# Kernel tuning notes

Hardware: AMD Instinct MI355X
Metric: run time of the kernel (lower is better)

The kernel has to match this reference:

```python
import jax, jax.numpy as jnp
import numpy as np

B, T, F, H = 512, 1024, 64, 512  # batch, timesteps, n_features, hidden_dims


def _lstm_cell(x, h, c, W_ih, W_hh, b_ih, b_hh):
    # torch.nn.LSTMCell gate order: i, f, g, o
    g = x @ W_ih.T + b_ih + h @ W_hh.T + b_hh
    i, f, gg, o = jnp.split(g, 4, axis=-1)
    c_new = jax.nn.sigmoid(f) * c + jax.nn.sigmoid(i) * jnp.tanh(gg)
    h_new = jax.nn.sigmoid(o) * jnp.tanh(c_new)
    return h_new, c_new


def setup_inputs() -> dict:
    key = jax.random.key(0)
    ks = jax.random.split(key, 9)
    s1 = 1.0 / np.sqrt(H)  # torch LSTMCell init scale for lstm1
    s2 = 1.0 / np.sqrt(F)  # for lstm2 (hidden size = n_features)
    u = lambda k, shape, s: jax.random.uniform(k, shape, jnp.float32, -s, s)
    return {
        "data": jax.random.normal(ks[0], (B, T * F), jnp.float32),
        "W_ih1": u(ks[1], (4 * H, F), s1),
        "W_hh1": u(ks[2], (4 * H, H), s1),
        "b_ih1": u(ks[3], (4 * H,), s1),
        "b_hh1": u(ks[4], (4 * H,), s1),
        "W_ih2": u(ks[5], (4 * F, H), s2),
        "W_hh2": u(ks[6], (4 * F, F), s2),
        "b_ih2": u(ks[7], (4 * F,), s2),
        "b_hh2": u(ks[8], (4 * F,), s2),
        "future": 0,
    }


def reference(data, W_ih1, W_hh1, b_ih1, b_hh1, W_ih2, W_hh2, b_ih2, b_hh2, future):
    x = data.reshape(B, T, F).transpose(1, 0, 2)  # [T, B, F] for scan
    h1 = jnp.zeros((B, H), data.dtype)
    c1 = jnp.zeros((B, H), data.dtype)
    h2 = jnp.zeros((B, F), data.dtype)
    c2 = jnp.zeros((B, F), data.dtype)  # this is the 'output' in the torch code

    def step(carry, x_t):
        h1, c1, h2, c2 = carry
        h1, c1 = _lstm_cell(x_t, h1, c1, W_ih1, W_hh1, b_ih1, b_hh1)
        # NOTE: original feeds c_t (cell state of lstm1) into lstm2, and the
        # per-step 'output' is lstm2's CELL state c2 (h_t2, output = lstm2(...)).
        h2, c2 = _lstm_cell(c1, h2, c2, W_ih2, W_hh2, b_ih2, b_hh2)
        return (h1, c1, h2, c2), c2

    (h1, c1, h2, c2), outs = jax.lax.scan(step, (h1, c1, h2, c2), x)
    outputs = [outs]  # [T, B, F]
    out_t = c2
    for _ in range(int(future)):  # future is a Python int constant
        h1, c1 = _lstm_cell(out_t, h1, c1, W_ih1, W_hh1, b_ih1, b_hh1)
        h2, out_t = _lstm_cell(c1, h2, out_t, W_ih2, W_hh2, b_ih2, b_hh2)
        outputs.append(out_t[None])
    out = jnp.concatenate(outputs, axis=0).transpose(1, 0, 2)  # [B, T+future, F]
    return jnp.squeeze(out, axis=2) if out.shape[2] == 1 else out
```

## Files before the change

### kernel.cpp

```cpp
#include <hip/hip_runtime.h>

#define Bn   512
#define Tn   1024
#define Fn   64
#define Hn   512
#define NB1  128
#define NB2  16
#define NBLK (NB1 + NB2)
#define GMEM 18
#define TRIES (1L << 22)

typedef short bf16x8 __attribute__((ext_vector_type(8)));
typedef float f32x4  __attribute__((ext_vector_type(4)));

__device__ __forceinline__ short f2bf(float f) {
    union { float f; unsigned u; } v; v.f = f;
    unsigned r = (v.u + 0x7FFFu + ((v.u >> 16) & 1u)) >> 16;
    return (short)(unsigned short)r;
}
__device__ __forceinline__ float sigm(float x) { return 1.f / (1.f + __expf(-x)); }
__device__ __forceinline__ float tanh_(float x) { return 2.f / (1.f + __expf(-2.f * x)) - 1.f; }

__device__ __forceinline__ bf16x8 cvt8(const float* p) {
    const float4 v0 = *(const float4*)p;
    const float4 v1 = *(const float4*)(p + 4);
    bf16x8 a;
    a[0] = f2bf(v0.x); a[1] = f2bf(v0.y); a[2] = f2bf(v0.z); a[3] = f2bf(v0.w);
    a[4] = f2bf(v1.x); a[5] = f2bf(v1.y); a[6] = f2bf(v1.z); a[7] = f2bf(v1.w);
    return a;
}

__device__ __forceinline__ void ldx16(bf16x8& d, const short* p) {
    asm volatile("global_load_dwordx4 %0, %1, off sc0 sc1" : "=v"(d) : "v"(p));
}
__device__ __forceinline__ void stx16(short* p, bf16x8 v) {
    asm volatile("global_store_dwordx4 %0, %1, off sc0 sc1" :: "v"(p), "v"(v) : "memory");
}
#define VMWAIT(N) do { \
    asm volatile("s_waitcnt vmcnt(" #N ")" ::: "memory"); \
    __builtin_amdgcn_sched_barrier(0); } while (0)

__device__ __forceinline__ int aldi(const int* p) {
    return __hip_atomic_load(p, __ATOMIC_RELAXED, __HIP_MEMORY_SCOPE_AGENT);
}

__device__ __forceinline__ void flag_arrive(int* slot, int val) {
    asm volatile("s_waitcnt vmcnt(0)" ::: "memory");
    __builtin_amdgcn_sched_barrier(0);
    __syncthreads();
    if (threadIdx.x == 0)
        __hip_atomic_store(slot, val, __ATOMIC_RELEASE, __HIP_MEMORY_SCOPE_AGENT);
}
__device__ __forceinline__ void flag_wait(const int* flags, int tgtA, int tgtB) {
    const int lane = threadIdx.x & 63;
    const int tgt = (lane < 16) ? tgtA : tgtB;
    long spins = 0;
    for (;;) {
        bool ok = (lane >= GMEM) ||
            (aldi(flags + lane) >= tgt);
        if (__all(ok)) break;
        if (++spins > TRIES) break;
        __builtin_amdgcn_s_sleep(1);
    }
    __atomic_signal_fence(__ATOMIC_ACQUIRE);
    __builtin_amdgcn_sched_barrier(0);
}

__global__ void prep_kernel(const float* __restrict__ Wih1, const float* __restrict__ Whh1,
                            const float* __restrict__ Wih2, const float* __restrict__ Whh2,
                            const float* __restrict__ bih1, const float* __restrict__ bhh1,
                            const float* __restrict__ bih2, const float* __restrict__ bhh2,
                            short* __restrict__ h1g, short* __restrict__ h2g,
                            short* __restrict__ w1f, short* __restrict__ w2f,
                            float* __restrict__ bs1, float* __restrict__ bs2,
                            int* __restrict__ bar) {
    const int i0 = blockIdx.x * blockDim.x + threadIdx.x;
    const int stride = gridDim.x * blockDim.x;
    for (int i = i0; i < 1024; i += stride) bar[i] = 0;
    for (int i = i0; i < 2 * Bn * Hn; i += stride) h1g[i] = 0;
    for (int i = i0; i < 2 * Bn * Fn; i += stride) h2g[i] = 0;
    for (int i = i0; i < 2048 * 576; i += stride) {
        int kk = i & 31, n = (i >> 5) & 15, ct = (i >> 9) & 3;
        int r = i >> 11; int kb = r % 18; int ut = r / 18;
        int gcol = ct * 512 + ut * 16 + n;
        int k = kb * 32 + kk;
        float v = (k < 64) ? Wih1[gcol * 64 + k] : Whh1[gcol * 512 + (k - 64)];
        w1f[i] = f2bf(v);
    }
    for (int i = i0; i < 256 * 576; i += stride) {
        int kk = i & 31, n = (i >> 5) & 15, ct = (i >> 9) & 3;
        int r = i >> 11; int kb = r % 18; int ut4 = r / 18;
        int gcol = ct * 64 + ut4 * 16 + n;
        int k = kb * 32 + kk;
        float v = (k < 512) ? Wih2[gcol * 512 + k] : Whh2[gcol * 64 + (k - 512)];
        w2f[i] = f2bf(v);
    }
    for (int i = i0; i < 2048; i += stride) bs1[i] = bih1[i] + bhh1[i];
    for (int i = i0; i < 256;  i += stride) bs2[i] = bih2[i] + bhh2[i];
}

__global__ __launch_bounds__(256, 1) void lstm_kernel(
    const float* __restrict__ data,
    const short* __restrict__ w1f, const float* __restrict__ bs1,
    const short* __restrict__ w2f, const float* __restrict__ bs2,
    short* __restrict__ h1g, short* __restrict__ c1g, short* __restrict__ h2g,
    float* __restrict__ out, int* __restrict__ bar) {
    extern __shared__ short smem[];
    const int tid = threadIdx.x;
    const int lane = tid & 63, wv = tid >> 6;
    const int n = lane & 15, q = lane >> 4;
    const int wvr = wv & 1, wvc = wv >> 1;
    const int bid = blockIdx.x;
    const f32x4 Z4 = {0.f, 0.f, 0.f, 0.f};
    short* htile = smem + 32768;
    short* ctile = smem + 34816;

    if (bid < NB1) {
        const int rt = bid >> 4, utp = bid & 15;
        const int ut = utp * 2 + wvc;
        const int rowbase = rt * 64 + wvr * 32;
        const int ucol = ut * 16 + n;
        int* grp = bar + rt * 32;
        const float bi_ = bs1[ucol], bf_ = bs1[512 + ucol], bg_ = bs1[1024 + ucol], bo_ = bs1[1536 + ucol];
        const short* wbase = w1f + ut * 36864 + n * 32 + q * 8;
        const int r0 = rowbase + n, r1 = rowbase + 16 + n;
        const int lr0 = wvr * 32 + n, lr1 = lr0 + 16, sw = n & 7;

        bf16x8 wr[16][4];
#pragma unroll
        for (int kb = 0; kb < 16; ++kb)
#pragma unroll
            for (int g = 0; g < 4; ++g)
                wr[kb][g] = *(const bf16x8*)(wbase + ((kb + 2) * 4 + g) * 512);

        f32x4 c1f[2]; c1f[0] = Z4; c1f[1] = Z4;

        for (int t = 0; t < Tn; ++t) {
            const short* h1r = h1g + (t & 1) * (Bn * Hn);
            short* h1w = h1g + ((t + 1) & 1) * (Bn * Hn);
            short* c1w = c1g + (t & 1) * (Bn * Hn);
            f32x4 acc[2][4];
#pragma unroll
            for (int a = 0; a < 2; ++a)
#pragma unroll
                for (int g = 0; g < 4; ++g) acc[a][g] = Z4;

            const float* x0 = data + (size_t)r0 * 65536 + t * 64;
            const float* x1 = data + (size_t)r1 * 65536 + t * 64;
#pragma unroll
            for (int kb = 0; kb < 2; ++kb) {
                const bf16x8 a0 = cvt8(x0 + kb * 32 + q * 8);
                const bf16x8 a1 = cvt8(x1 + kb * 32 + q * 8);
#pragma unroll
                for (int g = 0; g < 4; ++g) {
                    const bf16x8 b = *(const bf16x8*)(wbase + (kb * 4 + g) * 512);
                    acc[0][g] = __builtin_amdgcn_mfma_f32_16x16x32_bf16(a0, b, acc[0][g], 0, 0, 0);
                    acc[1][g] = __builtin_amdgcn_mfma_f32_16x16x32_bf16(a1, b, acc[1][g], 0, 0, 0);
                }
            }

            flag_wait(grp, t, t - 1);

            const short* gsrc = h1r + (size_t)rt * 32768;
            bf16x8 st[16];
            __builtin_amdgcn_sched_barrier(0);
#pragma unroll
            for (int i = 0; i < 16; ++i) {
                const int c = i * 256 + tid;
                ldx16(st[i], gsrc + c * 8);
            }
            VMWAIT(8);
#pragma unroll
            for (int i = 0; i < 8; ++i) {
                const int c = i * 256 + tid; const int row = c >> 6, col = c & 63;
                *(bf16x8*)&smem[row * 512 + ((col ^ (row & 7)) * 8)] = st[i];
            }
            VMWAIT(0);
#pragma unroll
            for (int i = 8; i < 16; ++i) {
                const int c = i * 256 + tid; const int row = c >> 6, col = c & 63;
                *(bf16x8*)&smem[row * 512 + ((col ^ (row & 7)) * 8)] = st[i];
            }
            __syncthreads();

#pragma unroll
            for (int kb = 0; kb < 16; ++kb) {
                const bf16x8 a0 = *(const bf16x8*)&smem[lr0 * 512 + (((kb * 4 + q) ^ sw) * 8)];
                const bf16x8 a1 = *(const bf16x8*)&smem[lr1 * 512 + (((kb * 4 + q) ^ sw) * 8)];
#pragma unroll
                for (int g = 0; g < 4; ++g) {
                    acc[0][g] = __builtin_amdgcn_mfma_f32_16x16x32_bf16(a0, wr[kb][g], acc[0][g], 0, 0, 0);
                    acc[1][g] = __builtin_amdgcn_mfma_f32_16x16x32_bf16(a1, wr[kb][g], acc[1][g], 0, 0, 0);
                }
            }

#pragma unroll
            for (int rt16 = 0; rt16 < 2; ++rt16) {
#pragma unroll
                for (int r = 0; r < 4; ++r) {
                    const float xi = acc[rt16][0][r] + bi_;
                    const float xf = acc[rt16][1][r] + bf_;
                    const float xg = acc[rt16][2][r] + bg_;
                    const float xo = acc[rt16][3][r] + bo_;
                    const float ii = sigm(xi), ff = sigm(xf), gg = tanh_(xg), oo = sigm(xo);
                    const float c = ff * c1f[rt16][r] + ii * gg;
                    c1f[rt16][r] = c;
                    const float h = oo * tanh_(c);
                    const int lr = wvr * 32 + rt16 * 16 + q * 4 + r;
                    const int lu = wvc * 16 + n;
                    htile[lr * 32 + lu] = f2bf(h);
                    ctile[lr * 32 + lu] = f2bf(c);
                }
            }
            __syncthreads();
            {
                const int row = tid >> 2, part = tid & 3;
                const bf16x8 hv = *(const bf16x8*)&htile[row * 32 + part * 8];
                const bf16x8 cv = *(const bf16x8*)&ctile[row * 32 + part * 8];
                short* gdst = h1w + (size_t)(rt * 64 + row) * 512 + utp * 32 + part * 8;
                short* gdc  = c1w + (size_t)(rt * 64 + row) * 512 + utp * 32 + part * 8;
                stx16(gdst, hv);
                stx16(gdc, cv);
            }
            flag_arrive(grp + utp, t + 1);
        }
    } else {
        const int b2 = bid - NB1;
        const int rt2 = b2 >> 1, u2 = b2 & 1;
        const int ut4 = u2 * 2 + wvc;
        const int rowbase = rt2 * 64 + wvr * 32;
        const int ucol = ut4 * 16 + n;
        int* grp = bar + rt2 * 32;
        const float bi_ = bs2[ucol], bf_ = bs2[64 + ucol], bg_ = bs2[128 + ucol], bo_ = bs2[192 + ucol];
        const short* wbase = w2f + ut4 * 36864 + n * 32 + q * 8;
        const int r0 = rowbase + n, r1 = rowbase + 16 + n;
        const int lr0 = wvr * 32 + n, lr1 = lr0 + 16, sw = n & 7;

        bf16x8 wr[16][4];
#pragma unroll
        for (int kb = 0; kb < 16; ++kb)
#pragma unroll
            for (int g = 0; g < 4; ++g)
                wr[kb][g] = *(const bf16x8*)(wbase + (kb * 4 + g) * 512);
        bf16x8 wh[2][4];
#pragma unroll
        for (int kb2 = 0; kb2 < 2; ++kb2)
#pragma unroll
            for (int g = 0; g < 4; ++g)
                wh[kb2][g] = *(const bf16x8*)(wbase + ((16 + kb2) * 4 + g) * 512);

        f32x4 c2f[2]; c2f[0] = Z4; c2f[1] = Z4;

        for (int t = 0; t < Tn; ++t) {
            flag_wait(grp, t + 1, t);
            const short* c1r = c1g + (t & 1) * (Bn * Hn);
            const short* h2r = h2g + (t & 1) * (Bn * Fn);
            short* h2w = h2g + ((t + 1) & 1) * (Bn * Fn);
            f32x4 acc[2][4];
#pragma unroll
            for (int a = 0; a < 2; ++a)
#pragma unroll
                for (int g = 0; g < 4; ++g) acc[a][g] = Z4;

            bf16x8 SH[4];
            __builtin_amdgcn_sched_barrier(0);
            ldx16(SH[0], h2r + (size_t)r0 * 64 + q * 8);
            ldx16(SH[1], h2r + (size_t)r0 * 64 + 32 + q * 8);
            ldx16(SH[2], h2r + (size_t)r1 * 64 + q * 8);
            ldx16(SH[3], h2r + (size_t)r1 * 64 + 32 + q * 8);
            const short* gsrc = c1r + (size_t)rt2 * 32768;
            bf16x8 st[16];
#pragma unroll
            for (int i = 0; i < 16; ++i) {
                const int c = i * 256 + tid;
                ldx16(st[i], gsrc + c * 8);
            }
            VMWAIT(8);
#pragma unroll
            for (int i = 0; i < 8; ++i) {
                const int c = i * 256 + tid; const int row = c >> 6, col = c & 63;
                *(bf16x8*)&smem[row * 512 + ((col ^ (row & 7)) * 8)] = st[i];
            }
            VMWAIT(0);
#pragma unroll
            for (int i = 8; i < 16; ++i) {
                const int c = i * 256 + tid; const int row = c >> 6, col = c & 7 ? (c & 63) : (c & 63);
                const int col2 = c & 63;
                *(bf16x8*)&smem[row * 512 + ((col2 ^ (row & 7)) * 8)] = st[i];
            }
            __syncthreads();

#pragma unroll
            for (int kb = 0; kb < 16; ++kb) {
                const bf16x8 a0 = *(const bf16x8*)&smem[lr0 * 512 + (((kb * 4 + q) ^ sw) * 8)];
                const bf16x8 a1 = *(const bf16x8*)&smem[lr1 * 512 + (((kb * 4 + q) ^ sw) * 8)];
#pragma unroll
                for (int g = 0; g < 4; ++g) {
                    acc[0][g] = __builtin_amdgcn_mfma_f32_16x16x32_bf16(a0, wr[kb][g], acc[0][g], 0, 0, 0);
                    acc[1][g] = __builtin_amdgcn_mfma_f32_16x16x32_bf16(a1, wr[kb][g], acc[1][g], 0, 0, 0);
                }
            }
#pragma unroll
            for (int g = 0; g < 4; ++g) {
                acc[0][g] = __builtin_amdgcn_mfma_f32_16x16x32_bf16(SH[0], wh[0][g], acc[0][g], 0, 0, 0);
                acc[0][g] = __builtin_amdgcn_mfma_f32_16x16x32_bf16(SH[1], wh[1][g], acc[0][g], 0, 0, 0);
                acc[1][g] = __builtin_amdgcn_mfma_f32_16x16x32_bf16(SH[2], wh[0][g], acc[1][g], 0, 0, 0);
                acc[1][g] = __builtin_amdgcn_mfma_f32_16x16x32_bf16(SH[3], wh[1][g], acc[1][g], 0, 0, 0);
            }

#pragma unroll
            for (int rt16 = 0; rt16 < 2; ++rt16) {
#pragma unroll
                for (int r = 0; r < 4; ++r) {
                    const float xi = acc[rt16][0][r] + bi_;
                    const float xf = acc[rt16][1][r] + bf_;
                    const float xg = acc[rt16][2][r] + bg_;
                    const float xo = acc[rt16][3][r] + bo_;
                    const float ii = sigm(xi), ff = sigm(xf), gg = tanh_(xg), oo = sigm(xo);
                    const float c = ff * c2f[rt16][r] + ii * gg;
                    c2f[rt16][r] = c;
                    const float h = oo * tanh_(c);
                    const int row = rowbase + rt16 * 16 + q * 4 + r;
                    out[(size_t)row * 65536 + (size_t)t * 64 + ucol] = c;
                    const int lr = wvr * 32 + rt16 * 16 + q * 4 + r;
                    const int lu = wvc * 16 + n;
                    htile[lr * 32 + lu] = f2bf(h);
                }
            }
            __syncthreads();
            {
                const int row = tid >> 2, part = tid & 3;
                const bf16x8 hv = *(const bf16x8*)&htile[row * 32 + part * 8];
                short* gdst = h2w + (size_t)(rt2 * 64 + row) * 64 + u2 * 32 + part * 8;
                stx16(gdst, hv);
            }
            flag_arrive(grp + 16 + u2, t + 1);
        }
    }
}

extern "C" void kernel_launch(void* const* d_in, const int* in_sizes, int n_in,
                              void* d_out, int out_size, void* d_ws, size_t ws_size,
                              hipStream_t stream) {
    const float* data = (const float*)d_in[0];
    const float* Wih1 = (const float*)d_in[1];
    const float* Whh1 = (const float*)d_in[2];
    const float* bih1 = (const float*)d_in[3];
    const float* bhh1 = (const float*)d_in[4];
    const float* Wih2 = (const float*)d_in[5];
    const float* Whh2 = (const float*)d_in[6];
    const float* bih2 = (const float*)d_in[7];
    const float* bhh2 = (const float*)d_in[8];
    float* out = (float*)d_out;

    char* w = (char*)d_ws;
    short* h1g = (short*)(w + 0);
    short* c1g = (short*)(w + 1048576);
    short* h2g = (short*)(w + 2097152);
    short* w2f = (short*)(w + 2228224);
    short* w1f = (short*)(w + 2523136);
    float* bs1 = (float*)(w + 4882432);
    float* bs2 = (float*)(w + 4890624);
    int* bar  = (int*)(w + 4891648);

    hipLaunchKernelGGL(prep_kernel, dim3(1024), dim3(256), 0, stream,
                       Wih1, Whh1, Wih2, Whh2, bih1, bhh1, bih2, bhh2,
                       h1g, h2g, w1f, w2f, bs1, bs2, bar);

    hipLaunchKernelGGL(lstm_kernel, dim3(NBLK), dim3(256), 73728, stream,
                       data, w1f, bs1, w2f, bs2, h1g, c1g, h2g, out, bar);
}
```

Before: 8.305 ms.

## Repartition LSTM blocks into 16 row groups of 9 with LDS-resident h2

Changes the block decomposition from 8 row groups of 64 rows (16 layer-1 blocks plus 2 layer-2 blocks each) to 16 groups of 32 rows, each with 8 layer-1 blocks and one layer-2 block. The layer-2 block now keeps its hidden state h2 in double-buffered shared memory instead of a global buffer, which removes the global h2 round trip and one internal barrier. Each group now synchronises through 9 flags instead of 18, and per-step h1/c1 tile loads are halved. The trade-off is smaller per-block tiles with the same total block count, and a single layer-2 block per group that handles all 64 output columns.

```diff
diff --git a/kernel.cpp b/kernel.cpp
--- a/kernel.cpp
+++ b/kernel.cpp
@@ -4,10 +4,9 @@
 #define Tn   1024
 #define Fn   64
 #define Hn   512
-#define NB1  128
-#define NB2  16
-#define NBLK (NB1 + NB2)
-#define GMEM 18
+#define NGRP 16
+#define GMEM 9
+#define NBLK (NGRP * GMEM)
 #define TRIES (1L << 22)
 
 typedef short bf16x8 __attribute__((ext_vector_type(8)));
@@ -53,11 +52,10 @@
 }
 __device__ __forceinline__ void flag_wait(const int* flags, int tgtA, int tgtB) {
     const int lane = threadIdx.x & 63;
-    const int tgt = (lane < 16) ? tgtA : tgtB;
+    const int tgt = (lane < 8) ? tgtA : tgtB;
     long spins = 0;
     for (;;) {
-        bool ok = (lane >= GMEM) ||
-            (aldi(flags + lane) >= tgt);
+        bool ok = (lane >= GMEM) || (aldi(flags + lane) >= tgt);
         if (__all(ok)) break;
         if (++spins > TRIES) break;
         __builtin_amdgcn_s_sleep(1);
@@ -103,28 +101,28 @@
     const float* __restrict__ data,
     const short* __restrict__ w1f, const float* __restrict__ bs1,
     const short* __restrict__ w2f, const float* __restrict__ bs2,
-    short* __restrict__ h1g, short* __restrict__ c1g, short* __restrict__ h2g,
+    short* __restrict__ h1g, short* __restrict__ c1g,
     float* __restrict__ out, int* __restrict__ bar) {
     extern __shared__ short smem[];
     const int tid = threadIdx.x;
     const int lane = tid & 63, wv = tid >> 6;
     const int n = lane & 15, q = lane >> 4;
-    const int wvr = wv & 1, wvc = wv >> 1;
+    const int wvc = wv;
     const int bid = blockIdx.x;
+    const int rt = bid / GMEM, role = bid % GMEM;
     const f32x4 Z4 = {0.f, 0.f, 0.f, 0.f};
-    short* htile = smem + 32768;
-    short* ctile = smem + 34816;
-
-    if (bid < NB1) {
-        const int rt = bid >> 4, utp = bid & 15;
-        const int ut = utp * 2 + wvc;
-        const int rowbase = rt * 64 + wvr * 32;
+    const int rowbase = rt * 32;
+    int* grp = bar + rt * 32;
+    short* tile0 = smem + 16384;
+    short* tile1 = smem + 18432;
+    const int r0 = rowbase + n, r1 = rowbase + 16 + n;
+    const int lr0 = n, lr1 = n + 16, sw = n & 7;
+
+    if (role < 8) {
+        const int ut = role * 4 + wvc;
         const int ucol = ut * 16 + n;
-        int* grp = bar + rt * 32;
         const float bi_ = bs1[ucol], bf_ = bs1[512 + ucol], bg_ = bs1[1024 + ucol], bo_ = bs1[1536 + ucol];
         const short* wbase = w1f + ut * 36864 + n * 32 + q * 8;
-        const int r0 = rowbase + n, r1 = rowbase + 16 + n;
-        const int lr0 = wvr * 32 + n, lr1 = lr0 + 16, sw = n & 7;
 
         bf16x8 wr[16][4];
 #pragma unroll
@@ -161,23 +159,20 @@
 
             flag_wait(grp, t, t - 1);
 
-            const short* gsrc = h1r + (size_t)rt * 32768;
-            bf16x8 st[16];
+            const short* gsrc = h1r + (size_t)rt * 16384;
+            bf16x8 st[8];
             __builtin_amdgcn_sched_barrier(0);
 #pragma unroll
-            for (int i = 0; i < 16; ++i) {
-                const int c = i * 256 + tid;
-                ldx16(st[i], gsrc + c * 8);
-            }
-            VMWAIT(8);
-#pragma unroll
-            for (int i = 0; i < 8; ++i) {
+            for (int i = 0; i < 8; ++i) ldx16(st[i], gsrc + (i * 256 + tid) * 8);
+            VMWAIT(4);
+#pragma unroll
+            for (int i = 0; i < 4; ++i) {
                 const int c = i * 256 + tid; const int row = c >> 6, col = c & 63;
                 *(bf16x8*)&smem[row * 512 + ((col ^ (row & 7)) * 8)] = st[i];
             }
             VMWAIT(0);
 #pragma unroll
-            for (int i = 8; i < 16; ++i) {
+            for (int i = 4; i < 8; ++i) {
                 const int c = i * 256 + tid; const int row = c >> 6, col = c & 63;
                 *(bf16x8*)&smem[row * 512 + ((col ^ (row & 7)) * 8)] = st[i];
             }
@@ -206,35 +201,29 @@
                     const float c = ff * c1f[rt16][r] + ii * gg;
                     c1f[rt16][r] = c;
                     const float h = oo * tanh_(c);
-                    const int lr = wvr * 32 + rt16 * 16 + q * 4 + r;
+                    const int lr = rt16 * 16 + q * 4 + r;
                     const int lu = wvc * 16 + n;
-                    htile[lr * 32 + lu] = f2bf(h);
-                    ctile[lr * 32 + lu] = f2bf(c);
+                    tile0[lr * 64 + lu] = f2bf(h);
+                    tile1[lr * 64 + lu] = f2bf(c);
                 }
             }
             __syncthreads();
             {
-                const int row = tid >> 2, part = tid & 3;
-                const bf16x8 hv = *(const bf16x8*)&htile[row * 32 + part * 8];
-                const bf16x8 cv = *(const bf16x8*)&ctile[row * 32 + part * 8];
-                short* gdst = h1w + (size_t)(rt * 64 + row) * 512 + utp * 32 + part * 8;
-                short* gdc  = c1w + (size_t)(rt * 64 + row) * 512 + utp * 32 + part * 8;
+                const int row = tid >> 3, part = tid & 7;
+                const bf16x8 hv = *(const bf16x8*)&tile0[row * 64 + part * 8];
+                const bf16x8 cv = *(const bf16x8*)&tile1[row * 64 + part * 8];
+                short* gdst = h1w + (size_t)(rowbase + row) * 512 + role * 64 + part * 8;
+                short* gdc  = c1w + (size_t)(rowbase + row) * 512 + role * 64 + part * 8;
                 stx16(gdst, hv);
                 stx16(gdc, cv);
             }
-            flag_arrive(grp + utp, t + 1);
+            flag_arrive(grp + role, t + 1);
         }
     } else {
-        const int b2 = bid - NB1;
-        const int rt2 = b2 >> 1, u2 = b2 & 1;
-        const int ut4 = u2 * 2 + wvc;
-        const int rowbase = rt2 * 64 + wvr * 32;
+        const int ut4 = wvc;
         const int ucol = ut4 * 16 + n;
-        int* grp = bar + rt2 * 32;
         const float bi_ = bs2[ucol], bf_ = bs2[64 + ucol], bg_ = bs2[128 + ucol], bo_ = bs2[192 + ucol];
         const short* wbase = w2f + ut4 * 36864 + n * 32 + q * 8;
-        const int r0 = rowbase + n, r1 = rowbase + 16 + n;
-        const int lr0 = wvr * 32 + n, lr1 = lr0 + 16, sw = n & 7;
 
         bf16x8 wr[16][4];
 #pragma unroll
@@ -249,44 +238,38 @@
             for (int g = 0; g < 4; ++g)
                 wh[kb2][g] = *(const bf16x8*)(wbase + ((16 + kb2) * 4 + g) * 512);
 
+        for (int i = tid; i < 2048; i += 256) { tile0[i] = 0; tile1[i] = 0; }
+        __syncthreads();
+
         f32x4 c2f[2]; c2f[0] = Z4; c2f[1] = Z4;
 
         for (int t = 0; t < Tn; ++t) {
             flag_wait(grp, t + 1, t);
             const short* c1r = c1g + (t & 1) * (Bn * Hn);
-            const short* h2r = h2g + (t & 1) * (Bn * Fn);
-            short* h2w = h2g + ((t + 1) & 1) * (Bn * Fn);
+            const short* h2rd = (t & 1) ? tile1 : tile0;
+            short* h2wr = (t & 1) ? tile0 : tile1;
             f32x4 acc[2][4];
 #pragma unroll
             for (int a = 0; a < 2; ++a)
 #pragma unroll
                 for (int g = 0; g < 4; ++g) acc[a][g] = Z4;
 
-            bf16x8 SH[4];
+            const short* gsrc = c1r + (size_t)rt * 16384;
+            bf16x8 st[8];
             __builtin_amdgcn_sched_barrier(0);
-            ldx16(SH[0], h2r + (size_t)r0 * 64 + q * 8);
-            ldx16(SH[1], h2r + (size_t)r0 * 64 + 32 + q * 8);
-            ldx16(SH[2], h2r + (size_t)r1 * 64 + q * 8);
-            ldx16(SH[3], h2r + (size_t)r1 * 64 + 32 + q * 8);
-            const short* gsrc = c1r + (size_t)rt2 * 32768;
-            bf16x8 st[16];
-#pragma unroll
-            for (int i = 0; i < 16; ++i) {
-                const int c = i * 256 + tid;
-                ldx16(st[i], gsrc + c * 8);
-            }
-            VMWAIT(8);
-#pragma unroll
-            for (int i = 0; i < 8; ++i) {
+#pragma unroll
+            for (int i = 0; i < 8; ++i) ldx16(st[i], gsrc + (i * 256 + tid) * 8);
+            VMWAIT(4);
+#pragma unroll
+            for (int i = 0; i < 4; ++i) {
                 const int c = i * 256 + tid; const int row = c >> 6, col = c & 63;
                 *(bf16x8*)&smem[row * 512 + ((col ^ (row & 7)) * 8)] = st[i];
             }
             VMWAIT(0);
 #pragma unroll
-            for (int i = 8; i < 16; ++i) {
-                const int c = i * 256 + tid; const int row = c >> 6, col = c & 7 ? (c & 63) : (c & 63);
-                const int col2 = c & 63;
-                *(bf16x8*)&smem[row * 512 + ((col2 ^ (row & 7)) * 8)] = st[i];
+            for (int i = 4; i < 8; ++i) {
+                const int c = i * 256 + tid; const int row = c >> 6, col = c & 63;
+                *(bf16x8*)&smem[row * 512 + ((col ^ (row & 7)) * 8)] = st[i];
             }
             __syncthreads();
 
@@ -301,11 +284,14 @@
                 }
             }
 #pragma unroll
-            for (int g = 0; g < 4; ++g) {
-                acc[0][g] = __builtin_amdgcn_mfma_f32_16x16x32_bf16(SH[0], wh[0][g], acc[0][g], 0, 0, 0);
-                acc[0][g] = __builtin_amdgcn_mfma_f32_16x16x32_bf16(SH[1], wh[1][g], acc[0][g], 0, 0, 0);
-                acc[1][g] = __builtin_amdgcn_mfma_f32_16x16x32_bf16(SH[2], wh[0][g], acc[1][g], 0, 0, 0);
-                acc[1][g] = __builtin_amdgcn_mfma_f32_16x16x32_bf16(SH[3], wh[1][g], acc[1][g], 0, 0, 0);
+            for (int kb2 = 0; kb2 < 2; ++kb2) {
+                const bf16x8 a0 = *(const bf16x8*)&h2rd[lr0 * 64 + (((kb2 * 4 + q) ^ sw) * 8)];
+                const bf16x8 a1 = *(const bf16x8*)&h2rd[lr1 * 64 + (((kb2 * 4 + q) ^ sw) * 8)];
+#pragma unroll
+                for (int g = 0; g < 4; ++g) {
+                    acc[0][g] = __builtin_amdgcn_mfma_f32_16x16x32_bf16(a0, wh[kb2][g], acc[0][g], 0, 0, 0);
+                    acc[1][g] = __builtin_amdgcn_mfma_f32_16x16x32_bf16(a1, wh[kb2][g], acc[1][g], 0, 0, 0);
+                }
             }
 
 #pragma unroll
@@ -320,21 +306,13 @@
                     const float c = ff * c2f[rt16][r] + ii * gg;
                     c2f[rt16][r] = c;
                     const float h = oo * tanh_(c);
-                    const int row = rowbase + rt16 * 16 + q * 4 + r;
-                    out[(size_t)row * 65536 + (size_t)t * 64 + ucol] = c;
-                    const int lr = wvr * 32 + rt16 * 16 + q * 4 + r;
+                    const int lr = rt16 * 16 + q * 4 + r;
                     const int lu = wvc * 16 + n;
-                    htile[lr * 32 + lu] = f2bf(h);
-                }
-            }
-            __syncthreads();
-            {
-                const int row = tid >> 2, part = tid & 3;
-                const bf16x8 hv = *(const bf16x8*)&htile[row * 32 + part * 8];
-                short* gdst = h2w + (size_t)(rt2 * 64 + row) * 64 + u2 * 32 + part * 8;
-                stx16(gdst, hv);
-            }
-            flag_arrive(grp + 16 + u2, t + 1);
+                    out[(size_t)(rowbase + lr) * 65536 + (size_t)t * 64 + ucol] = c;
+                    h2wr[lr * 64 + (((lu >> 3) ^ (lr & 7)) * 8) + (lu & 7)] = f2bf(h);
+                }
+            }
+            flag_arrive(grp + 8, t + 1);
         }
     }
 }
@@ -367,6 +345,6 @@
                        Wih1, Whh1, Wih2, Whh2, bih1, bhh1, bih2, bhh2,
                        h1g, h2g, w1f, w2f, bs1, bs2, bar);
 
-    hipLaunchKernelGGL(lstm_kernel, dim3(NBLK), dim3(256), 73728, stream,
-                       data, w1f, bs1, w2f, bs2, h1g, c1g, h2g, out, bar);
-}
+    hipLaunchKernelGGL(lstm_kernel, dim3(NBLK), dim3(256), 40960, stream,
+                       data, w1f, bs1, w2f, bs2, h1g, c1g, out, bar);
+}
```

After: 7.511 ms. -9.6%, faster.
